# Kernel tuning notes

Measured on AMD Instinct MI355X. Metric: run time of the kernel, lower is better.

## Reference

```python
import jax, jax.numpy as jnp
import numpy as np

N_HEAD = 16
NEG = -1e9


def setup_inputs() -> dict:
    key = jax.random.key(0)
    ks = jax.random.split(key, 10)
    b, s, f = 4, 1024, 1024
    h = N_HEAD
    scale = 1.0 / np.sqrt(f).astype(np.float32)
    x = jax.random.normal(ks[0], (b, s, f), jnp.float32)
    str_mat = jax.random.normal(ks[1], (b, h, s, s), jnp.float32)
    # causal binary mask, float as in the torch module (attn_mask == 0.0 test)
    attn_mask = jnp.broadcast_to(jnp.tril(jnp.ones((s, s), jnp.float32))[None, None], (b, 1, s, s))
    Wq = jax.random.normal(ks[2], (f, f), jnp.float32) * scale
    Wk = jax.random.normal(ks[3], (f, f), jnp.float32) * scale
    Wv = jax.random.normal(ks[4], (f, f), jnp.float32) * scale
    Wo = jax.random.normal(ks[5], (f, f), jnp.float32) * scale
    bq = jax.random.normal(ks[6], (f,), jnp.float32) * 0.01
    bk = jax.random.normal(ks[7], (f,), jnp.float32) * 0.01
    bv = jax.random.normal(ks[8], (f,), jnp.float32) * 0.01
    bo = jax.random.normal(ks[9], (f,), jnp.float32) * 0.01
    return {"x": x, "str_mat": str_mat, "attn_mask": attn_mask,
            "Wq": Wq, "bq": bq, "Wk": Wk, "bk": bk,
            "Wv": Wv, "bv": bv, "Wo": Wo, "bo": bo}


def reference(x, str_mat, attn_mask, Wq, bq, Wk, bk, Wv, bv, Wo, bo):
    b, s, f = x.shape
    h = N_HEAD
    d_h = f // h
    # NOTE: original uses .view(b, h, -1, d_h) with NO transpose -> raw reshape
    q = (x @ Wq + bq).reshape(b, h, s, d_h)
    k = (x @ Wk + bk).reshape(b, h, s, d_h)
    v = (x @ Wv + bv).reshape(b, h, s, d_h)
    # structural bias: mask then softmax
    sm = jnp.where(attn_mask == 0.0, NEG, str_mat)
    sm = jax.nn.softmax(sm, axis=-1)
    # scale by d_h (NOT sqrt(d_h)) as in source; second masked_fill in source
    # is non-in-place with result discarded -> no-op, intentionally omitted
    scores = jnp.einsum('bhqd,bhkd->bhqk', q, k) / d_h + sm
    prob = jax.nn.softmax(scores, axis=-1)  # dropout p=0.0
    out = jnp.einsum('bhqk,bhkd->bhqd', prob, v)  # [b,h,s,d_h]
    out = out.transpose(0, 2, 1, 3).reshape(b, s, f)
    return out @ Wo + bo
```

## Files before the change

### kernel.cpp

```cpp
#include <hip/hip_runtime.h>
#include <hip/hip_bf16.h>

#define BB 4
#define SS 1024
#define FF 1024
#define HH 16
#define DH 64

typedef short bf16x8 __attribute__((ext_vector_type(8)));
typedef float f32x4 __attribute__((ext_vector_type(4)));

__device__ __forceinline__ float b2f(unsigned short u) {
    union { unsigned int i; float f; } x; x.i = ((unsigned int)u) << 16; return x.f;
}
__device__ __forceinline__ unsigned short f2b(float f) {
    unsigned int x = __float_as_uint(f);
    unsigned int r = (x + 0x7fffu + ((x >> 16) & 1u)) >> 16;
    return (unsigned short)r;
}

__global__ void cvt_k(const float* __restrict__ in, unsigned short* __restrict__ out, int n) {
    int i = (blockIdx.x * blockDim.x + threadIdx.x) * 4;
    if (i < n) {
        float4 v = *(const float4*)(in + i);
        ushort4 o;
        o.x = f2b(v.x); o.y = f2b(v.y); o.z = f2b(v.z); o.w = f2b(v.w);
        *(ushort4*)(out + i) = o;
    }
}

__global__ void cvtT_k(const float* __restrict__ W0, const float* __restrict__ W1,
                       const float* __restrict__ W2, const float* __restrict__ W3,
                       unsigned short* __restrict__ out) {
    int y = blockIdx.y;
    const float* src = (y == 0) ? W0 : (y == 1) ? W1 : (y == 2) ? W2 : W3;
    unsigned short* dst = out + (size_t)y * FF * FF;
    __shared__ float t[32][33];
    int tile = blockIdx.x;
    int tk = (tile & 31) * 32, tn = (tile >> 5) * 32;
    int r = threadIdx.x >> 3, c4 = (threadIdx.x & 7) * 4;
    float4 v = *(const float4*)&src[(size_t)(tk + r) * FF + tn + c4];
    t[r][c4 + 0] = v.x; t[r][c4 + 1] = v.y; t[r][c4 + 2] = v.z; t[r][c4 + 3] = v.w;
    __syncthreads();
    ushort4 o;
    o.x = f2b(t[c4 + 0][r]); o.y = f2b(t[c4 + 1][r]);
    o.z = f2b(t[c4 + 2][r]); o.w = f2b(t[c4 + 3][r]);
    *(ushort4*)&dst[(size_t)(tn + r) * FF + tk + c4] = o;
}

__global__ void vtrans_k(const unsigned short* __restrict__ V, unsigned short* __restrict__ Vt) {
    int bh = blockIdx.y;
    int sb = blockIdx.x * 64;
    size_t slab = (size_t)bh * SS * DH;
    __shared__ unsigned int tI[64][65];
    int tid = threadIdx.x;
    #pragma unroll
    for (int v = 0; v < 2; v++) {
        int c = tid + v * 256;
        int row = c >> 3, col = (c & 7) * 8;
        uint4 u = *(const uint4*)&V[slab + (size_t)(sb + row) * DH + col];
        const unsigned short* us = (const unsigned short*)&u;
        #pragma unroll
        for (int j = 0; j < 8; j++) tI[row][col + j] = us[j];
    }
    __syncthreads();
    #pragma unroll
    for (int v = 0; v < 2; v++) {
        int c = tid + v * 256;
        int drow = c >> 3, scol = (c & 7) * 8;
        unsigned short o[8];
        #pragma unroll
        for (int j = 0; j < 8; j++) o[j] = (unsigned short)tI[scol + j][drow];
        *(uint4*)&Vt[slab + (size_t)drow * SS + sb + scol] = *(uint4*)o;
    }
}

#define LDK 72
__global__ __launch_bounds__(256, 1) void gemm_k(
    const unsigned short* __restrict__ A, const unsigned short* __restrict__ Wt,
    const float* __restrict__ bias,
    unsigned short* __restrict__ o16, float* __restrict__ o32, float scale, int mode)
{
    __shared__ __attribute__((aligned(16))) unsigned short lA[2][128 * LDK];
    __shared__ __attribute__((aligned(16))) unsigned short lB[2][128 * LDK];

    int tid = threadIdx.x;
    int wave = tid >> 6, lane = tid & 63, quad = lane >> 4, l16 = lane & 15;
    int wm = (wave & 1) * 64, wn = (wave >> 1) * 64;
    int mbase = blockIdx.x * 128, nbase = blockIdx.y * 128;
    int srow = tid >> 3, scol = (tid & 7) * 8;

    f32x4 acc[4][4];
    #pragma unroll
    for (int i = 0; i < 4; i++)
        #pragma unroll
        for (int j = 0; j < 4; j++) acc[i][j] = (f32x4){0.f, 0.f, 0.f, 0.f};

    const unsigned short* pA = A  + (size_t)(mbase + srow) * FF + scol;
    const unsigned short* pB = Wt + (size_t)(nbase + srow) * FF + scol;

    uint4 ra[4], rb[4];
    #pragma unroll
    for (int i = 0; i < 4; i++) {
        ra[i] = *(const uint4*)(pA + (size_t)i * 32 * FF);
        rb[i] = *(const uint4*)(pB + (size_t)i * 32 * FF);
    }
    #pragma unroll
    for (int i = 0; i < 4; i++) {
        *(uint4*)&lA[0][(srow + i * 32) * LDK + scol] = ra[i];
        *(uint4*)&lB[0][(srow + i * 32) * LDK + scol] = rb[i];
    }
    __syncthreads();

    for (int kt = 0; kt < 16; kt++) {
        int cur = kt & 1;
        if (kt < 15) {
            #pragma unroll
            for (int i = 0; i < 4; i++) {
                ra[i] = *(const uint4*)(pA + (kt + 1) * 64 + (size_t)i * 32 * FF);
                rb[i] = *(const uint4*)(pB + (kt + 1) * 64 + (size_t)i * 32 * FF);
            }
        }
        #pragma unroll
        for (int ks = 0; ks < 2; ks++) {
            bf16x8 af[4], bfr[4];
            #pragma unroll
            for (int mi = 0; mi < 4; mi++)
                af[mi] = *(const bf16x8*)(&lA[cur][(wm + mi * 16 + l16) * LDK + ks * 32 + quad * 8]);
            #pragma unroll
            for (int ni = 0; ni < 4; ni++)
                bfr[ni] = *(const bf16x8*)(&lB[cur][(wn + ni * 16 + l16) * LDK + ks * 32 + quad * 8]);
            #pragma unroll
            for (int mi = 0; mi < 4; mi++)
                #pragma unroll
                for (int ni = 0; ni < 4; ni++)
                    acc[mi][ni] = __builtin_amdgcn_mfma_f32_16x16x32_bf16(af[mi], bfr[ni], acc[mi][ni], 0, 0, 0);
        }
        if (kt < 15) {
            #pragma unroll
            for (int i = 0; i < 4; i++) {
                *(uint4*)&lA[cur ^ 1][(srow + i * 32) * LDK + scol] = ra[i];
                *(uint4*)&lB[cur ^ 1][(srow + i * 32) * LDK + scol] = rb[i];
            }
        }
        __syncthreads();
    }

    #pragma unroll
    for (int mi = 0; mi < 4; mi++) {
        #pragma unroll
        for (int ni = 0; ni < 4; ni++) {
            int col = nbase + wn + ni * 16 + l16;
            float bv = bias[col];
            #pragma unroll
            for (int r = 0; r < 4; r++) {
                int row = mbase + wm + mi * 16 + quad * 4 + r;
                float v = (acc[mi][ni][r] + bv) * scale;
                if (mode == 1) {
                    int b_ = row >> 10, i = row & 1023;
                    int h = i >> 6, s_ = ((i & 63) << 4) + (col >> 6), d = col & 63;
                    o16[(((size_t)(b_ * HH + h)) * SS + s_) * DH + d] = f2b(v);
                } else {
                    o32[(size_t)row * FF + col] = v;
                }
            }
        }
    }
}

__global__ void rowstats_k(const float* __restrict__ str,
                           float* __restrict__ rmax, float* __restrict__ rinv) {
    int row = blockIdx.x * 4 + (threadIdx.x >> 6);
    int lane = threadIdx.x & 63;
    int r = row & (SS - 1);
    const float* p = str + (size_t)row * SS;
    float vals[16];
    float mx = -1e30f;
    #pragma unroll
    for (int i = 0; i < 4; i++) {
        int k0 = i * 256 + lane * 4;
        float4 u = *(const float4*)(&p[k0]);
        float uv[4] = {u.x, u.y, u.z, u.w};
        #pragma unroll
        for (int j = 0; j < 4; j++) {
            float v = (k0 + j <= r) ? uv[j] : -1e30f;
            vals[i * 4 + j] = v;
            mx = fmaxf(mx, v);
        }
    }
    #pragma unroll
    for (int d = 1; d < 64; d <<= 1) mx = fmaxf(mx, __shfl_xor(mx, d));
    float sum = 0.f;
    #pragma unroll
    for (int i = 0; i < 16; i++) sum += __expf(fminf(vals[i] - mx, 0.f));
    #pragma unroll
    for (int d = 1; d < 64; d <<= 1) sum += __shfl_xor(sum, d);
    if (lane == 0) { rmax[row] = mx; rinv[row] = 1.0f / sum; }
}

#define LDT 72
__global__ __launch_bounds__(256, 2) void attn_k(
    const unsigned short* __restrict__ Q, const unsigned short* __restrict__ K,
    const unsigned short* __restrict__ Vt, const float* __restrict__ str,
    const float* __restrict__ rmax, const float* __restrict__ rinv,
    unsigned short* __restrict__ ctx)
{
    int bh = blockIdx.y;
    int b_ = bh >> 4, h = bh & 15;
    int qbase = blockIdx.x * 64;
    int tid = threadIdx.x;
    int wave = tid >> 6, lane = tid & 63, quad = lane >> 4, l16 = lane & 15;
    int srow = tid >> 3, scol = (tid & 7) * 8;

    __shared__ __attribute__((aligned(16))) unsigned short lQP[64 * LDT];
    __shared__ __attribute__((aligned(16))) unsigned short lK[2][64 * LDT];
    __shared__ __attribute__((aligned(16))) unsigned short lV[2][64 * LDT];

    const size_t slab = (size_t)bh * SS * DH;

    #pragma unroll
    for (int v = 0; v < 2; v++) {
        int row = srow + v * 32;
        *(uint4*)&lQP[row * LDT + scol]   = *(const uint4*)&Q [slab + (size_t)(qbase + row) * DH + scol];
        *(uint4*)&lK[0][row * LDT + scol] = *(const uint4*)&K [slab + (size_t)row * DH + scol];
        *(uint4*)&lV[0][row * LDT + scol] = *(const uint4*)&Vt[slab + (size_t)row * SS + scol];
    }
    int q_loc0 = wave * 16 + quad * 4;
    float rm4[4], ri4[4];
    #pragma unroll
    for (int r = 0; r < 4; r++) {
        rm4[r] = rmax[bh * SS + qbase + q_loc0 + r];
        ri4[r] = rinv[bh * SS + qbase + q_loc0 + r];
    }
    __syncthreads();

    bf16x8 aq[2];
    #pragma unroll
    for (int ks = 0; ks < 2; ks++)
        aq[ks] = *(const bf16x8*)&lQP[(wave * 16 + l16) * LDT + ks * 32 + quad * 8];

    float m_st[4], l_st[4];
    f32x4 Oacc[4];
    #pragma unroll
    for (int r = 0; r < 4; r++) { m_st[r] = -1e30f; l_st[r] = 0.f; }
    #pragma unroll
    for (int ni = 0; ni < 4; ni++) Oacc[ni] = (f32x4){0.f, 0.f, 0.f, 0.f};

    const size_t strbase = (size_t)bh * SS * SS;
    unsigned short* lPw = &lQP[(wave * 16) * LDT];

    for (int tt = 0; tt < 16; tt++) {
        int cur = tt & 1;
        int tbase = tt * 64;
        bool need_sm = (tbase <= qbase + 63);

        float sf[4][4];
        if (need_sm) {
            #pragma unroll
            for (int r = 0; r < 4; r++) {
                int q_abs = qbase + q_loc0 + r;
                int lim = q_abs - tbase;
                const float* pr = str + strbase + (size_t)q_abs * SS + tbase + l16;
                #pragma unroll
                for (int ni = 0; ni < 4; ni++)
                    sf[ni][r] = (ni * 16 + l16 <= lim) ? pr[ni * 16] : -1e30f;
            }
        }
        uint4 kst[2], vst[2];
        if (tt < 15) {
            #pragma unroll
            for (int v = 0; v < 2; v++) {
                int row = srow + v * 32;
                kst[v] = *(const uint4*)&K [slab + (size_t)(tbase + 64 + row) * DH + scol];
                vst[v] = *(const uint4*)&Vt[slab + (size_t)row * SS + tbase + 64 + scol];
            }
        }

        f32x4 sa[4];
        #pragma unroll
        for (int ni = 0; ni < 4; ni++) sa[ni] = (f32x4){0.f, 0.f, 0.f, 0.f};
        #pragma unroll
        for (int ks = 0; ks < 2; ks++) {
            #pragma unroll
            for (int ni = 0; ni < 4; ni++) {
                bf16x8 bk_ = *(const bf16x8*)&lK[cur][(ni * 16 + l16) * LDT + ks * 32 + quad * 8];
                sa[ni] = __builtin_amdgcn_mfma_f32_16x16x32_bf16(aq[ks], bk_, sa[ni], 0, 0, 0);
            }
        }

        float tm[4];
        #pragma unroll
        for (int r = 0; r < 4; r++) tm[r] = -1e30f;
        #pragma unroll
        for (int ni = 0; ni < 4; ni++) {
            #pragma unroll
            for (int r = 0; r < 4; r++) {
                float v = sa[ni][r];
                if (need_sm)
                    v += __expf(fminf(sf[ni][r] - rm4[r], 0.f)) * ri4[r];
                sa[ni][r] = v;
                tm[r] = fmaxf(tm[r], v);
            }
        }
        #pragma unroll
        for (int r = 0; r < 4; r++) {
            float v = tm[r];
            v = fmaxf(v, __shfl_xor(v, 1));
            v = fmaxf(v, __shfl_xor(v, 2));
            v = fmaxf(v, __shfl_xor(v, 4));
            v = fmaxf(v, __shfl_xor(v, 8));
            tm[r] = v;
        }
        float alpha[4], rs[4];
        #pragma unroll
        for (int r = 0; r < 4; r++) {
            float mn = fmaxf(m_st[r], tm[r]);
            alpha[r] = __expf(fminf(m_st[r] - mn, 0.f));
            m_st[r] = mn;
            rs[r] = 0.f;
        }
        #pragma unroll
        for (int ni = 0; ni < 4; ni++)
            #pragma unroll
            for (int r = 0; r < 4; r++) {
                sa[ni][r] = __expf(fminf(sa[ni][r] - m_st[r], 0.f));
                rs[r] += sa[ni][r];
            }
        #pragma unroll
        for (int r = 0; r < 4; r++) {
            float v = rs[r];
            v += __shfl_xor(v, 1); v += __shfl_xor(v, 2);
            v += __shfl_xor(v, 4); v += __shfl_xor(v, 8);
            l_st[r] = l_st[r] * alpha[r] + v;
        }
        #pragma unroll
        for (int ni = 0; ni < 4; ni++)
            #pragma unroll
            for (int r = 0; r < 4; r++) Oacc[ni][r] *= alpha[r];

        #pragma unroll
        for (int ni = 0; ni < 4; ni++)
            #pragma unroll
            for (int r = 0; r < 4; r++)
                lPw[(quad * 4 + r) * LDT + ni * 16 + l16] = f2b(sa[ni][r]);

        #pragma unroll
        for (int ks = 0; ks < 2; ks++) {
            bf16x8 pa = *(const bf16x8*)&lPw[l16 * LDT + ks * 32 + quad * 8];
            #pragma unroll
            for (int ni = 0; ni < 4; ni++) {
                bf16x8 bv = *(const bf16x8*)&lV[cur][(ni * 16 + l16) * LDT + ks * 32 + quad * 8];
                Oacc[ni] = __builtin_amdgcn_mfma_f32_16x16x32_bf16(pa, bv, Oacc[ni], 0, 0, 0);
            }
        }

        if (tt < 15) {
            #pragma unroll
            for (int v = 0; v < 2; v++) {
                int row = srow + v * 32;
                *(uint4*)&lK[cur ^ 1][row * LDT + scol] = kst[v];
                *(uint4*)&lV[cur ^ 1][row * LDT + scol] = vst[v];
            }
        }
        __syncthreads();
    }

    #pragma unroll
    for (int r = 0; r < 4; r++) {
        int s_abs = qbase + wave * 16 + quad * 4 + r;
        float li = 1.0f / l_st[r];
        #pragma unroll
        for (int ni = 0; ni < 4; ni++) {
            int d = ni * 16 + l16;
            ctx[((size_t)b_ * SS + s_abs) * FF + h * 64 + d] = f2b(Oacc[ni][r] * li);
        }
    }
}

extern "C" void kernel_launch(void* const* d_in, const int* in_sizes, int n_in,
                              void* d_out, int out_size, void* d_ws, size_t ws_size,
                              hipStream_t stream) {
    const float* x   = (const float*)d_in[0];
    const float* str = (const float*)d_in[1];
    const float* Wq  = (const float*)d_in[3];
    const float* bq  = (const float*)d_in[4];
    const float* Wk  = (const float*)d_in[5];
    const float* bk  = (const float*)d_in[6];
    const float* Wv  = (const float*)d_in[7];
    const float* bv  = (const float*)d_in[8];
    const float* Wo  = (const float*)d_in[9];
    const float* bo  = (const float*)d_in[10];

    char* ws = (char*)d_ws;
    const size_t MB = 1024ull * 1024;
    unsigned short* xb  = (unsigned short*)ws;
    unsigned short* Wb  = (unsigned short*)(ws + 8 * MB);
    unsigned short* QKV = (unsigned short*)(ws + 16 * MB);
    unsigned short* Vtp = (unsigned short*)(ws + 40 * MB);
    unsigned short* ctx = (unsigned short*)(ws + 48 * MB);
    float* rmax = (float*)(ws + 56 * MB);
    float* rinv = (float*)(ws + 56 * MB + 256 * 1024);

    const size_t QN = (size_t)BB * SS * FF;
    const size_t WN = (size_t)FF * FF;

    cvt_k<<<4096, 256, 0, stream>>>(x, xb, (int)QN);
    cvtT_k<<<dim3(1024, 4), 256, 0, stream>>>(Wq, Wk, Wv, Wo, Wb);

    gemm_k<<<dim3(32, 8), 256, 0, stream>>>(xb, Wb,          bq, QKV,          nullptr, 0.015625f, 1);
    gemm_k<<<dim3(32, 8), 256, 0, stream>>>(xb, Wb + WN,     bk, QKV + QN,     nullptr, 1.0f,      1);
    gemm_k<<<dim3(32, 8), 256, 0, stream>>>(xb, Wb + 2 * WN, bv, QKV + 2 * QN, nullptr, 1.0f,      1);
    vtrans_k<<<dim3(16, 64), 256, 0, stream>>>(QKV + 2 * QN, Vtp);
    rowstats_k<<<16384, 256, 0, stream>>>(str, rmax, rinv);
    attn_k<<<dim3(16, 64), 256, 0, stream>>>(QKV, QKV + QN, Vtp, str, rmax, rinv, ctx);
    gemm_k<<<dim3(32, 8), 256, 0, stream>>>(ctx, Wb + 3 * WN, bo, nullptr, (float*)d_out, 1.0f, 0);
}
```

Measured before the change: 587.3 us.

## Swizzle LDS tiles instead of padding and merge QKV GEMMs into one launch

Replaces padded shared-memory rows (stride 72) with unpadded 64-wide tiles using an XOR swizzle on 8-element chunks in both the GEMM and attention kernels. The three Q/K/V projection GEMMs are merged into a single launch whose grid y-dimension selects the weight, bias, scale and output. This aims to cut launch overhead and reduce LDS footprint and bank conflicts, at the cost of extra index arithmetic and per-block selection logic.

```diff
diff --git a/kernel.cpp b/kernel.cpp
--- a/kernel.cpp
+++ b/kernel.cpp
@@ -18,6 +18,7 @@
     unsigned int r = (x + 0x7fffu + ((x >> 16) & 1u)) >> 16;
     return (unsigned short)r;
 }
+__device__ __forceinline__ int sw(int row, int col) { return col ^ ((row & 7) << 3); }
 
 __global__ void cvt_k(const float* __restrict__ in, unsigned short* __restrict__ out, int n) {
     int i = (blockIdx.x * blockDim.x + threadIdx.x) * 4;
@@ -75,29 +76,45 @@
     }
 }
 
-#define LDK 72
 __global__ __launch_bounds__(256, 1) void gemm_k(
     const unsigned short* __restrict__ A, const unsigned short* __restrict__ Wt,
-    const float* __restrict__ bias,
-    unsigned short* __restrict__ o16, float* __restrict__ o32, float scale, int mode)
+    const float* __restrict__ b0, const float* __restrict__ b1, const float* __restrict__ b2,
+    unsigned short* __restrict__ o16, float* __restrict__ o32, int mode)
 {
-    __shared__ __attribute__((aligned(16))) unsigned short lA[2][128 * LDK];
-    __shared__ __attribute__((aligned(16))) unsigned short lB[2][128 * LDK];
+    __shared__ __attribute__((aligned(16))) unsigned short lA[2][128 * 64];
+    __shared__ __attribute__((aligned(16))) unsigned short lB[2][128 * 64];
 
     int tid = threadIdx.x;
     int wave = tid >> 6, lane = tid & 63, quad = lane >> 4, l16 = lane & 15;
     int wm = (wave & 1) * 64, wn = (wave >> 1) * 64;
-    int mbase = blockIdx.x * 128, nbase = blockIdx.y * 128;
+    int mbase = blockIdx.x * 128;
     int srow = tid >> 3, scol = (tid & 7) * 8;
 
+    int nbase;
+    const float* bias;
+    float scale = 1.0f;
+    const unsigned short* W = Wt;
+    unsigned short* oq = o16;
+    if (mode == 1) {
+        int widx = blockIdx.y >> 3;
+        nbase = (blockIdx.y & 7) * 128;
+        W = Wt + (size_t)widx * FF * FF;
+        bias = (widx == 0) ? b0 : (widx == 1) ? b1 : b2;
+        scale = (widx == 0) ? 0.015625f : 1.0f;
+        oq = o16 + (size_t)widx * BB * SS * FF;
+    } else {
+        nbase = blockIdx.y * 128;
+        bias = b0;
+    }
+
     f32x4 acc[4][4];
     #pragma unroll
     for (int i = 0; i < 4; i++)
         #pragma unroll
         for (int j = 0; j < 4; j++) acc[i][j] = (f32x4){0.f, 0.f, 0.f, 0.f};
 
-    const unsigned short* pA = A  + (size_t)(mbase + srow) * FF + scol;
-    const unsigned short* pB = Wt + (size_t)(nbase + srow) * FF + scol;
+    const unsigned short* pA = A + (size_t)(mbase + srow) * FF + scol;
+    const unsigned short* pB = W + (size_t)(nbase + srow) * FF + scol;
 
     uint4 ra[4], rb[4];
     #pragma unroll
@@ -107,8 +124,8 @@
     }
     #pragma unroll
     for (int i = 0; i < 4; i++) {
-        *(uint4*)&lA[0][(srow + i * 32) * LDK + scol] = ra[i];
-        *(uint4*)&lB[0][(srow + i * 32) * LDK + scol] = rb[i];
+        *(uint4*)&lA[0][(srow + i * 32) * 64 + sw(srow, scol)] = ra[i];
+        *(uint4*)&lB[0][(srow + i * 32) * 64 + sw(srow, scol)] = rb[i];
     }
     __syncthreads();
 
@@ -125,11 +142,15 @@
         for (int ks = 0; ks < 2; ks++) {
             bf16x8 af[4], bfr[4];
             #pragma unroll
-            for (int mi = 0; mi < 4; mi++)
-                af[mi] = *(const bf16x8*)(&lA[cur][(wm + mi * 16 + l16) * LDK + ks * 32 + quad * 8]);
-            #pragma unroll
-            for (int ni = 0; ni < 4; ni++)
-                bfr[ni] = *(const bf16x8*)(&lB[cur][(wn + ni * 16 + l16) * LDK + ks * 32 + quad * 8]);
+            for (int mi = 0; mi < 4; mi++) {
+                int row = wm + mi * 16 + l16;
+                af[mi] = *(const bf16x8*)(&lA[cur][row * 64 + sw(row, ks * 32 + quad * 8)]);
+            }
+            #pragma unroll
+            for (int ni = 0; ni < 4; ni++) {
+                int row = wn + ni * 16 + l16;
+                bfr[ni] = *(const bf16x8*)(&lB[cur][row * 64 + sw(row, ks * 32 + quad * 8)]);
+            }
             #pragma unroll
             for (int mi = 0; mi < 4; mi++)
                 #pragma unroll
@@ -139,8 +160,8 @@
         if (kt < 15) {
             #pragma unroll
             for (int i = 0; i < 4; i++) {
-                *(uint4*)&lA[cur ^ 1][(srow + i * 32) * LDK + scol] = ra[i];
-                *(uint4*)&lB[cur ^ 1][(srow + i * 32) * LDK + scol] = rb[i];
+                *(uint4*)&lA[cur ^ 1][(srow + i * 32) * 64 + sw(srow, scol)] = ra[i];
+                *(uint4*)&lB[cur ^ 1][(srow + i * 32) * 64 + sw(srow, scol)] = rb[i];
             }
         }
         __syncthreads();
@@ -159,7 +180,7 @@
                 if (mode == 1) {
                     int b_ = row >> 10, i = row & 1023;
                     int h = i >> 6, s_ = ((i & 63) << 4) + (col >> 6), d = col & 63;
-                    o16[(((size_t)(b_ * HH + h)) * SS + s_) * DH + d] = f2b(v);
+                    oq[(((size_t)(b_ * HH + h)) * SS + s_) * DH + d] = f2b(v);
                 } else {
                     o32[(size_t)row * FF + col] = v;
                 }
@@ -198,7 +219,6 @@
     if (lane == 0) { rmax[row] = mx; rinv[row] = 1.0f / sum; }
 }
 
-#define LDT 72
 __global__ __launch_bounds__(256, 2) void attn_k(
     const unsigned short* __restrict__ Q, const unsigned short* __restrict__ K,
     const unsigned short* __restrict__ Vt, const float* __restrict__ str,
@@ -212,18 +232,18 @@
     int wave = tid >> 6, lane = tid & 63, quad = lane >> 4, l16 = lane & 15;
     int srow = tid >> 3, scol = (tid & 7) * 8;
 
-    __shared__ __attribute__((aligned(16))) unsigned short lQP[64 * LDT];
-    __shared__ __attribute__((aligned(16))) unsigned short lK[2][64 * LDT];
-    __shared__ __attribute__((aligned(16))) unsigned short lV[2][64 * LDT];
+    __shared__ __attribute__((aligned(16))) unsigned short lQP[64 * 64];
+    __shared__ __attribute__((aligned(16))) unsigned short lK[2][64 * 64];
+    __shared__ __attribute__((aligned(16))) unsigned short lV[2][64 * 64];
 
     const size_t slab = (size_t)bh * SS * DH;
 
     #pragma unroll
     for (int v = 0; v < 2; v++) {
         int row = srow + v * 32;
-        *(uint4*)&lQP[row * LDT + scol]   = *(const uint4*)&Q [slab + (size_t)(qbase + row) * DH + scol];
-        *(uint4*)&lK[0][row * LDT + scol] = *(const uint4*)&K [slab + (size_t)row * DH + scol];
-        *(uint4*)&lV[0][row * LDT + scol] = *(const uint4*)&Vt[slab + (size_t)row * SS + scol];
+        *(uint4*)&lQP[row * 64 + sw(row, scol)]   = *(const uint4*)&Q [slab + (size_t)(qbase + row) * DH + scol];
+        *(uint4*)&lK[0][row * 64 + sw(row, scol)] = *(const uint4*)&K [slab + (size_t)row * DH + scol];
+        *(uint4*)&lV[0][row * 64 + sw(row, scol)] = *(const uint4*)&Vt[slab + (size_t)row * SS + scol];
     }
     int q_loc0 = wave * 16 + quad * 4;
     float rm4[4], ri4[4];
@@ -236,8 +256,10 @@
 
     bf16x8 aq[2];
     #pragma unroll
-    for (int ks = 0; ks < 2; ks++)
-        aq[ks] = *(const bf16x8*)&lQP[(wave * 16 + l16) * LDT + ks * 32 + quad * 8];
+    for (int ks = 0; ks < 2; ks++) {
+        int row = wave * 16 + l16;
+        aq[ks] = *(const bf16x8*)&lQP[row * 64 + sw(row, ks * 32 + quad * 8)];
+    }
 
     float m_st[4], l_st[4];
     f32x4 Oacc[4];
@@ -247,7 +269,7 @@
     for (int ni = 0; ni < 4; ni++) Oacc[ni] = (f32x4){0.f, 0.f, 0.f, 0.f};
 
     const size_t strbase = (size_t)bh * SS * SS;
-    unsigned short* lPw = &lQP[(wave * 16) * LDT];
+    unsigned short* lPw = &lQP[(wave * 16) * 64];
 
     for (int tt = 0; tt < 16; tt++) {
         int cur = tt & 1;
@@ -283,7 +305,8 @@
         for (int ks = 0; ks < 2; ks++) {
             #pragma unroll
             for (int ni = 0; ni < 4; ni++) {
-                bf16x8 bk_ = *(const bf16x8*)&lK[cur][(ni * 16 + l16) * LDT + ks * 32 + quad * 8];
+                int row = ni * 16 + l16;
+                bf16x8 bk_ = *(const bf16x8*)&lK[cur][row * 64 + sw(row, ks * 32 + quad * 8)];
                 sa[ni] = __builtin_amdgcn_mfma_f32_16x16x32_bf16(aq[ks], bk_, sa[ni], 0, 0, 0);
             }
         }
@@ -341,15 +364,18 @@
         #pragma unroll
         for (int ni = 0; ni < 4; ni++)
             #pragma unroll
-            for (int r = 0; r < 4; r++)
-                lPw[(quad * 4 + r) * LDT + ni * 16 + l16] = f2b(sa[ni][r]);
+            for (int r = 0; r < 4; r++) {
+                int pr = quad * 4 + r;
+                lPw[pr * 64 + sw(pr, ni * 16 + l16)] = f2b(sa[ni][r]);
+            }
 
         #pragma unroll
         for (int ks = 0; ks < 2; ks++) {
-            bf16x8 pa = *(const bf16x8*)&lPw[l16 * LDT + ks * 32 + quad * 8];
+            bf16x8 pa = *(const bf16x8*)&lPw[l16 * 64 + sw(l16, ks * 32 + quad * 8)];
             #pragma unroll
             for (int ni = 0; ni < 4; ni++) {
-                bf16x8 bv = *(const bf16x8*)&lV[cur][(ni * 16 + l16) * LDT + ks * 32 + quad * 8];
+                int row = ni * 16 + l16;
+                bf16x8 bv = *(const bf16x8*)&lV[cur][row * 64 + sw(row, ks * 32 + quad * 8)];
                 Oacc[ni] = __builtin_amdgcn_mfma_f32_16x16x32_bf16(pa, bv, Oacc[ni], 0, 0, 0);
             }
         }
@@ -358,8 +384,8 @@
             #pragma unroll
             for (int v = 0; v < 2; v++) {
                 int row = srow + v * 32;
-                *(uint4*)&lK[cur ^ 1][row * LDT + scol] = kst[v];
-                *(uint4*)&lV[cur ^ 1][row * LDT + scol] = vst[v];
+                *(uint4*)&lK[cur ^ 1][row * 64 + sw(row, scol)] = kst[v];
+                *(uint4*)&lV[cur ^ 1][row * 64 + sw(row, scol)] = vst[v];
             }
         }
         __syncthreads();
@@ -407,11 +433,9 @@
     cvt_k<<<4096, 256, 0, stream>>>(x, xb, (int)QN);
     cvtT_k<<<dim3(1024, 4), 256, 0, stream>>>(Wq, Wk, Wv, Wo, Wb);
 
-    gemm_k<<<dim3(32, 8), 256, 0, stream>>>(xb, Wb,          bq, QKV,          nullptr, 0.015625f, 1);
-    gemm_k<<<dim3(32, 8), 256, 0, stream>>>(xb, Wb + WN,     bk, QKV + QN,     nullptr, 1.0f,      1);
-    gemm_k<<<dim3(32, 8), 256, 0, stream>>>(xb, Wb + 2 * WN, bv, QKV + 2 * QN, nullptr, 1.0f,      1);
+    gemm_k<<<dim3(32, 24), 256, 0, stream>>>(xb, Wb, bq, bk, bv, QKV, nullptr, 1);
     vtrans_k<<<dim3(16, 64), 256, 0, stream>>>(QKV + 2 * QN, Vtp);
     rowstats_k<<<16384, 256, 0, stream>>>(str, rmax, rinv);
     attn_k<<<dim3(16, 64), 256, 0, stream>>>(QKV, QKV + QN, Vtp, str, rmax, rinv, ctx);
-    gemm_k<<<dim3(32, 8), 256, 0, stream>>>(ctx, Wb + 3 * WN, bo, nullptr, (float*)d_out, 1.0f, 0);
-}
+    gemm_k<<<dim3(32, 8), 256, 0, stream>>>(ctx, Wb + 3 * WN, bo, nullptr, nullptr, nullptr, (float*)d_out, 0);
+}
```

Measured after the change: 557.1 us. -5.1%, faster.
